# Optimization experiments

Measured on AMD Instinct MI355X. Metric: run time of the kernel, lower is better.

## Reference

```python
import jax, jax.numpy as jnp
import numpy as np
from jax.scipy.linalg import expm

D = 512      # d_model
S = 3        # num_scales
BATCH = 256
H = 8        # attention heads
HD = D // H  # head dim


def layernorm(x, g, b, eps=1e-5):
    m = jnp.mean(x, axis=-1, keepdims=True)
    v = jnp.var(x, axis=-1, keepdims=True)
    return (x - m) / jnp.sqrt(v + eps) * g + b


def setup_inputs() -> dict:
    key = jax.random.key(0)
    ks = jax.random.split(key, 16)
    sd = 1.0 / np.sqrt(D)
    inp = {
        'x': jax.random.normal(ks[0], (BATCH, D), jnp.float32),
        'h_prev': jax.random.normal(ks[1], (BATCH, D), jnp.float32),
        'lstm_h': jax.random.normal(ks[2], (S, BATCH, D), jnp.float32) * 0.1,
        'lstm_c': jax.random.normal(ks[3], (S, BATCH, D), jnp.float32) * 0.1,
        'A': jax.random.normal(ks[4], (D, D), jnp.float32) * sd,
        'Bm': jax.random.normal(ks[5], (D, D), jnp.float32) * sd,
        'dn_w1': jax.random.normal(ks[6], (D, D), jnp.float32) * sd,
        'dn_b1': jnp.zeros((D,), jnp.float32),
        'dn_g': jnp.ones((D,), jnp.float32),
        'dn_beta': jnp.zeros((D,), jnp.float32),
        'dn_w2': jax.random.normal(ks[7], (1, D), jnp.float32) * sd,
        'dn_b2': jnp.zeros((1,), jnp.float32),
        'lstm_wih': jax.random.normal(ks[8], (S, 4 * D, D), jnp.float32) * sd,
        'lstm_whh': jax.random.normal(ks[9], (S, 4 * D, D), jnp.float32) * sd,
        'lstm_bih': jnp.zeros((S, 4 * D), jnp.float32),
        'lstm_bhh': jnp.zeros((S, 4 * D), jnp.float32),
        'decays': jnp.linspace(0.5, 0.95, S, dtype=jnp.float32),
        'attn_in_w': jax.random.normal(ks[10], (3 * D, D), jnp.float32) * sd,
        'attn_in_b': jnp.zeros((3 * D,), jnp.float32),
        'attn_out_w': jax.random.normal(ks[11], (D, D), jnp.float32) * sd,
        'attn_out_b': jnp.zeros((D,), jnp.float32),
        'proj_w': jax.random.normal(ks[12], (D, (S + 2) * D), jnp.float32) * (1.0 / np.sqrt((S + 2) * D)),
        'proj_b': jnp.zeros((D,), jnp.float32),
        'proj_g': jnp.ones((D,), jnp.float32),
        'proj_beta': jnp.zeros((D,), jnp.float32),
    }
    return inp


def reference(x, h_prev, lstm_h, lstm_c, A, Bm, dn_w1, dn_b1, dn_g, dn_beta,
              dn_w2, dn_b2, lstm_wih, lstm_whh, lstm_bih, lstm_bhh, decays,
              attn_in_w, attn_in_b, attn_out_w, attn_out_b,
              proj_w, proj_b, proj_g, proj_beta):
    # ---- delta_net: Linear -> LayerNorm -> GELU(exact) -> Linear -> Softplus ----
    h1 = layernorm(x @ dn_w1.T + dn_b1, dn_g, dn_beta)
    h1 = jax.nn.gelu(h1, approximate=False)
    delta = jax.nn.softplus(h1 @ dn_w2.T + dn_b2)           # (B, 1)

    # ---- SSM update: h_t = expm(delta*A) h_prev + delta*B x ----
    A_disc = jax.vmap(expm)(delta[:, :, None] * A)          # (B, D, D)
    h_ssm = jnp.einsum('bij,bj->bi', A_disc, h_prev) + delta * jnp.einsum('ij,bj->bi', Bm, x)

    # ---- multi-scale LSTM cells (vectorized over scales) ----
    gates = (jnp.einsum('bd,skd->sbk', x, lstm_wih)
             + jnp.einsum('sbd,skd->sbk', lstm_h, lstm_whh)
             + (lstm_bih + lstm_bhh)[:, None, :])           # (S, B, 4D)
    gi, gf, gg, go = jnp.split(gates, 4, axis=-1)
    i_g = jax.nn.sigmoid(gi)
    f_g = jax.nn.sigmoid(gf)
    g_g = jnp.tanh(gg)
    o_g = jax.nn.sigmoid(go)
    c_raw = f_g * lstm_c + i_g * g_g                        # (S, B, D)
    h_new = o_g * jnp.tanh(c_raw)                           # (S, B, D)
    dec = decays[:, None, None]
    c_new = dec * lstm_c + (1.0 - dec) * c_raw              # (S, B, D)

    # ---- fusion attention: 1 query (h_ssm), S keys/values (h_new) ----
    Wq, Wk, Wv = jnp.split(attn_in_w, 3, axis=0)
    bq, bk, bv = jnp.split(attn_in_b, 3, axis=0)
    kv = jnp.transpose(h_new, (1, 0, 2))                    # (B, S, D)
    q = (h_ssm @ Wq.T + bq).reshape(-1, 1, H, HD).transpose(0, 2, 1, 3)   # (B,H,1,HD)
    k = (kv @ Wk.T + bk).reshape(-1, S, H, HD).transpose(0, 2, 1, 3)      # (B,H,S,HD)
    v = (kv @ Wv.T + bv).reshape(-1, S, H, HD).transpose(0, 2, 1, 3)
    scores = jnp.einsum('bhqe,bhke->bhqk', q, k) / np.sqrt(HD)
    attn = jax.nn.softmax(scores, axis=-1)
    ctx = jnp.einsum('bhqk,bhke->bhqe', attn, v)            # (B,H,1,HD)
    ctx = ctx.transpose(0, 2, 1, 3).reshape(-1, D)          # (B, D)
    fused = ctx @ attn_out_w.T + attn_out_b                 # (B, D)

    # ---- output projection over concat [h_ssm, fused, h_1..h_S] ----
    combined = jnp.concatenate([h_ssm, fused] + [h_new[i] for i in range(S)], axis=-1)
    output = layernorm(combined @ proj_w.T + proj_b, proj_g, proj_beta)
    return (output, h_ssm, h_new, c_new)
```

## Files before the change

kernel.cpp:

```cpp
#include <hip/hip_runtime.h>
#include <math.h>

#define DIM 512
#define NB 256
#define KMAX 12

using bf16x8 = __attribute__((ext_vector_type(8))) short;
using f32x4  = __attribute__((ext_vector_type(4))) float;
using float4v = __attribute__((ext_vector_type(4))) float;
using ushort4v = __attribute__((ext_vector_type(4))) unsigned short;

__device__ __forceinline__ unsigned short f2b(float f) {
    union { float f; unsigned int u; } v; v.f = f;
    unsigned int r = v.u + 0x7fffu + ((v.u >> 16) & 1u);
    return (unsigned short)(r >> 16);
}
__device__ __forceinline__ float b2f(unsigned short u) {
    union { unsigned int u; float f; } v; v.u = ((unsigned int)u) << 16;
    return v.f;
}
__device__ __forceinline__ ushort4v f2b4(float4v v) {
    ushort4v o;
    o.x = f2b(v.x); o.y = f2b(v.y); o.z = f2b(v.z); o.w = f2b(v.w);
    return o;
}

__device__ __forceinline__ void block_reduce2(float& s, float& q, float* sb1, float* sb2)
{
    int tid = threadIdx.x;
    #pragma unroll
    for (int off = 32; off > 0; off >>= 1) {
        s += __shfl_down(s, off);
        q += __shfl_down(q, off);
    }
    if ((tid & 63) == 0) { sb1[tid >> 6] = s; sb2[tid >> 6] = q; }
    __syncthreads();
    s = sb1[0] + sb1[1] + sb1[2] + sb1[3];
    q = sb2[0] + sb2[1] + sb2[2] + sb2[3];
    __syncthreads();
}

struct GemmDesc {
    const unsigned short* X;
    const unsigned short* W;
    const float* bias;
    float* Cf;
    unsigned short* Cb;
    unsigned short* Ct;
    int M, N, K, ldX, ldW, ldC, tr_row0, acc;
};
struct GemmArgs { GemmDesc d[10]; };
struct LnParams {
    const float* pre; const float* g; const float* beta;
    const float* w2; const float* b2; float* delta; float* coeff;
    int lnd_y;
};

__global__ __launch_bounds__(256) void gemm_mfma(GemmArgs args, LnParams lp)
{
    __shared__ unsigned short lsA[2][8192];
    __shared__ unsigned short lsB[2][8192];
    __shared__ float sb1[4], sb2[4];

    if ((int)blockIdx.y == lp.lnd_y) {
        int b = blockIdx.x, tid = threadIdx.x;
        int i0 = tid, i1 = tid + 256;
        float x0 = lp.pre[(size_t)b * DIM + i0];
        float x1 = lp.pre[(size_t)b * DIM + i1];
        float s = x0 + x1, q = x0 * x0 + x1 * x1;
        block_reduce2(s, q, sb1, sb2);
        float mean = s * (1.f / DIM);
        float var  = q * (1.f / DIM) - mean * mean;
        float inv  = rsqrtf(var + 1e-5f);
        float y0 = (x0 - mean) * inv * lp.g[i0] + lp.beta[i0];
        float y1 = (x1 - mean) * inv * lp.g[i1] + lp.beta[i1];
        float h0 = 0.5f * y0 * (1.f + erff(y0 * 0.70710678118654752f));
        float h1 = 0.5f * y1 * (1.f + erff(y1 * 0.70710678118654752f));
        float p = h0 * lp.w2[i0] + h1 * lp.w2[i1];
        float dummy = 0.f;
        block_reduce2(p, dummy, sb1, sb2);
        if (tid == 0) {
            float z = p + lp.b2[0];
            float d = (z > 20.f) ? z : log1pf(expf(z));
            lp.delta[b] = d;
            float c = 1.f;
            lp.coeff[b] = 1.f;
            for (int k = 1; k <= KMAX; ++k) { c *= d / (float)k; lp.coeff[k * 256 + b] = c; }
        }
        return;
    }

    GemmDesc de = args.d[blockIdx.y];
    int tn = de.N >> 6;
    int tiles = (de.M >> 6) * tn;
    int t = blockIdx.x;
    if (t >= tiles) return;
    int m0 = (t / tn) << 6;
    int n0 = (t % tn) << 6;

    int tid = threadIdx.x;
    int w = tid >> 6;
    int l = tid & 63;
    int nkt = de.K >> 7;

    int srow = w * 16 + (l >> 2);
    int schk = l & 3;
    const unsigned short* gA = de.X + (size_t)(m0 + srow) * de.ldX + schk * 8;
    const unsigned short* gB = de.W + (size_t)(n0 + srow) * de.ldW + schk * 8;
    unsigned short* lA = &lsA[0][(w * 64 + l) * 8];
    unsigned short* lB = &lsB[0][(w * 64 + l) * 8];

#define STAGE(bufi, kt)                                                          \
    do {                                                                         \
        for (int hh = 0; hh < 4; ++hh) {                                         \
            __builtin_amdgcn_global_load_lds(                                    \
                (const __attribute__((address_space(1))) unsigned int*)(gA + (size_t)(kt) * 128 + hh * 32), \
                (__attribute__((address_space(3))) unsigned int*)(lA + (bufi) * 8192 + hh * 2048), 16, 0, 0); \
            __builtin_amdgcn_global_load_lds(                                    \
                (const __attribute__((address_space(1))) unsigned int*)(gB + (size_t)(kt) * 128 + hh * 32), \
                (__attribute__((address_space(3))) unsigned int*)(lB + (bufi) * 8192 + hh * 2048), 16, 0, 0); \
        }                                                                        \
    } while (0)

    int mbase = (w >> 1) * 32;
    int nbase = (w & 1) * 32;

    f32x4 acc[2][2];
    #pragma unroll
    for (int i = 0; i < 2; ++i)
        #pragma unroll
        for (int j = 0; j < 2; ++j)
            acc[i][j] = (f32x4){0.f, 0.f, 0.f, 0.f};

    int kg = l >> 4;
    int fr = l & 15;
    int aslot = (mbase * 4 + fr * 4 + kg) * 8;
    int bslot = (nbase * 4 + fr * 4 + kg) * 8;

    STAGE(0, 0);

    for (int kt = 0; kt < nkt; ++kt) {
        __syncthreads();
        if (kt + 1 < nkt) STAGE((kt + 1) & 1, kt + 1);

        const unsigned short* bufA = &lsA[kt & 1][0];
        const unsigned short* bufB = &lsB[kt & 1][0];
        #pragma unroll
        for (int h = 0; h < 4; ++h) {
            bf16x8 a0 = *(const bf16x8*)(bufA + h * 2048 + aslot);
            bf16x8 a1 = *(const bf16x8*)(bufA + h * 2048 + aslot + 512);
            bf16x8 b0 = *(const bf16x8*)(bufB + h * 2048 + bslot);
            bf16x8 b1 = *(const bf16x8*)(bufB + h * 2048 + bslot + 512);
            acc[0][0] = __builtin_amdgcn_mfma_f32_16x16x32_bf16(a0, b0, acc[0][0], 0, 0, 0);
            acc[0][1] = __builtin_amdgcn_mfma_f32_16x16x32_bf16(a0, b1, acc[0][1], 0, 0, 0);
            acc[1][0] = __builtin_amdgcn_mfma_f32_16x16x32_bf16(a1, b0, acc[1][0], 0, 0, 0);
            acc[1][1] = __builtin_amdgcn_mfma_f32_16x16x32_bf16(a1, b1, acc[1][1], 0, 0, 0);
        }
    }

    #pragma unroll
    for (int mi = 0; mi < 2; ++mi) {
        #pragma unroll
        for (int ni = 0; ni < 2; ++ni) {
            int col = n0 + nbase + ni * 16 + fr;
            float bv = de.bias ? de.bias[col] : 0.f;
            #pragma unroll
            for (int r = 0; r < 4; ++r) {
                int row = m0 + mbase + mi * 16 + (l >> 4) * 4 + r;
                float v = acc[mi][ni][r] + bv;
                if (de.Cf) {
                    if (de.acc == 2)      atomicAdd(&de.Cf[(size_t)row * de.ldC + col], v);
                    else if (de.acc == 1) de.Cf[(size_t)row * de.ldC + col] += v;
                    else                  de.Cf[(size_t)row * de.ldC + col] = v;
                } else {
                    de.Cb[(size_t)row * de.ldC + col] = f2b(v);
                }
                if (de.Ct && row >= de.tr_row0)
                    de.Ct[(size_t)col * 512 + (row - de.tr_row0)] = f2b(v);
            }
        }
    }
#undef STAGE
}

#define NSEG 13
struct PrepArgs {
    const float* sA[NSEG]; const float* sB[NSEG]; unsigned short* dst[NSEG];
    int n4[NSEG], dRL4[NSEG], sRLA4[NSEG], sRLB4[NSEG], half4[NSEG], offA[NSEG];
    const float* A; unsigned short* ATb;
    const float* W2src; unsigned short* W2dst;
};
__global__ __launch_bounds__(256) void prep_kernel(PrepArgs a)
{
    __shared__ float tile[32][33];
    int bid = blockIdx.x, tid = threadIdx.x;
    if (bid < 2048) {
        const int gstride = 2048 * 256;
        int g0 = bid * 256 + tid;
        for (int seg = 0; seg < NSEG; ++seg) {
            int n4 = a.n4[seg];
            const float* sA = a.sA[seg];
            const float* sB = a.sB[seg];
            unsigned short* d = a.dst[seg];
            int dRL4 = a.dRL4[seg], sRLA4 = a.sRLA4[seg], sRLB4 = a.sRLB4[seg];
            int half4 = a.half4[seg], offA = a.offA[seg];
            for (int i = g0; i < n4; i += gstride) {
                int r = i / dRL4, c = i - r * dRL4;
                const float* src = (c < half4)
                    ? sA + ((size_t)r * sRLA4 + offA + c) * 4
                    : sB + ((size_t)r * sRLB4 + (c - half4)) * 4;
                float4v v = *(const float4v*)src;
                *(ushort4v*)(d + (size_t)i * 4) = f2b4(v);
            }
        }
    } else {
        int tt = bid - 2048;
        const float* src = a.A;
        unsigned short* dst = a.ATb;
        if (tt >= 256) { tt -= 256; src = a.W2src; dst = a.W2dst; }
        int bx = tt & 15, by = tt >> 4;
        int tx = tid & 31, ty = tid >> 5;
        #pragma unroll
        for (int i = 0; i < 32; i += 8)
            tile[ty + i][tx] = src[(size_t)(by * 32 + ty + i) * 512 + bx * 32 + tx];
        __syncthreads();
        #pragma unroll
        for (int i = 0; i < 32; i += 8)
            dst[(size_t)(bx * 32 + ty + i) * 512 + by * 32 + tx] = f2b(tile[tx][ty + i]);
    }
}

__global__ void pointwise_fused(
    const float* __restrict__ Tm, const float* __restrict__ coeff,
    const float* __restrict__ h_prev, const float* __restrict__ delta,
    const float* __restrict__ Bx, float* __restrict__ hssm,
    unsigned short* __restrict__ combb,
    const float* __restrict__ gates, const float* __restrict__ bih,
    const float* __restrict__ bhh, const float* __restrict__ cin,
    const float* __restrict__ decays,
    float* __restrict__ hout, float* __restrict__ cout,
    const unsigned short* __restrict__ P2b, const float* __restrict__ aout_b,
    const float* __restrict__ proj_b, float* __restrict__ pbc)
{
    int idx4 = blockIdx.x * 256 + threadIdx.x;
    int base = idx4 * 4;
    if (base < 131072) {
        int b = base >> 9, i = base & 511;
        const float* Tr = Tm + (size_t)b * (KMAX * DIM) + i;
        float4v a = *(const float4v*)(h_prev + base);
        #pragma unroll
        for (int k = 1; k <= KMAX; ++k) {
            float c = coeff[k * 256 + b];
            float4v t = *(const float4v*)(Tr + (size_t)(k - 1) * DIM);
            a.x += c * t.x; a.y += c * t.y; a.z += c * t.z; a.w += c * t.w;
        }
        float dl = delta[b];
        float4v bx = *(const float4v*)(Bx + base);
        a.x += dl * bx.x; a.y += dl * bx.y; a.z += dl * bx.z; a.w += dl * bx.w;
        *(float4v*)(hssm + base) = a;
        *(ushort4v*)(combb + (size_t)b * 2048 + i) = f2b4(a);
    } else if (base < 524288) {
        int i2 = base - 131072;
        int s = i2 / (NB * DIM);
        int r = i2 - s * (NB * DIM);
        int b = r >> 9, d = r & 511;
        const float* gr = gates + (size_t)s * 524288 + (size_t)b * 2048 + d;
        const float* bi = bih + s * 2048 + d;
        const float* bh = bhh + s * 2048 + d;
        float4v gi = *(const float4v*)(gr);
        float4v gf = *(const float4v*)(gr + 512);
        float4v gg = *(const float4v*)(gr + 1024);
        float4v go = *(const float4v*)(gr + 1536);
        float4v bi0 = *(const float4v*)(bi),        bh0 = *(const float4v*)(bh);
        float4v bi1 = *(const float4v*)(bi + 512),  bh1 = *(const float4v*)(bh + 512);
        float4v bi2 = *(const float4v*)(bi + 1024), bh2 = *(const float4v*)(bh + 1024);
        float4v bi3 = *(const float4v*)(bi + 1536), bh3 = *(const float4v*)(bh + 1536);
        float4v c = *(const float4v*)(cin + i2);
        float dec = decays[s];
        float4v hn, cn;
        #pragma unroll
        for (int j = 0; j < 4; ++j) {
            float vgi = ((const float*)&gi)[j] + ((const float*)&bi0)[j] + ((const float*)&bh0)[j];
            float vgf = ((const float*)&gf)[j] + ((const float*)&bi1)[j] + ((const float*)&bh1)[j];
            float vgg = ((const float*)&gg)[j] + ((const float*)&bi2)[j] + ((const float*)&bh2)[j];
            float vgo = ((const float*)&go)[j] + ((const float*)&bi3)[j] + ((const float*)&bh3)[j];
            float ig = 1.f / (1.f + expf(-vgi));
            float fg = 1.f / (1.f + expf(-vgf));
            float g_ = tanhf(vgg);
            float og = 1.f / (1.f + expf(-vgo));
            float cc = ((const float*)&c)[j];
            float craw = fg * cc + ig * g_;
            ((float*)&hn)[j] = og * tanhf(craw);
            ((float*)&cn)[j] = dec * cc + (1.f - dec) * craw;
        }
        *(float4v*)(hout + i2) = hn;
        *(float4v*)(cout + i2) = cn;
        *(ushort4v*)(combb + (size_t)b * 2048 + 512 + s * 512 + d) = f2b4(hn);
    } else {
        int ii = idx4 - 131072;
        const unsigned short* pr = P2b + (size_t)ii * 512;
        float acc = 0.f;
        for (int k = 0; k < 512; k += 8) {
            ushort4v w0 = *(const ushort4v*)(pr + k);
            ushort4v w1 = *(const ushort4v*)(pr + k + 4);
            float4v a0 = *(const float4v*)(aout_b + k);
            float4v a1 = *(const float4v*)(aout_b + k + 4);
            acc += a0.x * b2f(w0.x) + a0.y * b2f(w0.y)
                 + a0.z * b2f(w0.z) + a0.w * b2f(w0.w)
                 + a1.x * b2f(w1.x) + a1.y * b2f(w1.y)
                 + a1.z * b2f(w1.z) + a1.w * b2f(w1.w);
        }
        pbc[ii] = proj_b[ii] + acc;
    }
}

__global__ __launch_bounds__(256) void tail_kernel(
    const unsigned short* __restrict__ qb, const unsigned short* __restrict__ kvb,
    const unsigned short* __restrict__ M2b, const float* __restrict__ projA,
    const float* __restrict__ fin_g, const float* __restrict__ fin_beta,
    float* __restrict__ outp)
{
    __shared__ float ctxs[512];
    __shared__ float sb1[4], sb2[4];
    int b = blockIdx.x, tid = threadIdx.x;

    if (tid < 128) {
        int h = tid >> 4, sub = (tid & 15) * 4;
        int col = h * 64 + sub;
        ushort4v q4 = *(const ushort4v*)(qb + (size_t)b * 512 + col);
        float qf[4] = { b2f(q4.x), b2f(q4.y), b2f(q4.z), b2f(q4.w) };
        float p[3];
        ushort4v k4[3], v4[3];
        #pragma unroll
        for (int s = 0; s < 3; ++s) {
            k4[s] = *(const ushort4v*)(kvb + (size_t)s * 262144 + (size_t)b * 1024 + col);
            v4[s] = *(const ushort4v*)(kvb + (size_t)s * 262144 + (size_t)b * 1024 + 512 + col);
            p[s] = qf[0] * b2f(k4[s].x) + qf[1] * b2f(k4[s].y)
                 + qf[2] * b2f(k4[s].z) + qf[3] * b2f(k4[s].w);
        }
        #pragma unroll
        for (int off = 1; off < 16; off <<= 1) {
            p[0] += __shfl_xor(p[0], off);
            p[1] += __shfl_xor(p[1], off);
            p[2] += __shfl_xor(p[2], off);
        }
        const float scale = 0.125f;
        float p0 = p[0] * scale, p1 = p[1] * scale, p2 = p[2] * scale;
        float m = fmaxf(p0, fmaxf(p1, p2));
        float w0 = expf(p0 - m), w1 = expf(p1 - m), w2 = expf(p2 - m);
        float invs = 1.f / (w0 + w1 + w2);
        ctxs[col + 0] = (w0 * b2f(v4[0].x) + w1 * b2f(v4[1].x) + w2 * b2f(v4[2].x)) * invs;
        ctxs[col + 1] = (w0 * b2f(v4[0].y) + w1 * b2f(v4[1].y) + w2 * b2f(v4[2].y)) * invs;
        ctxs[col + 2] = (w0 * b2f(v4[0].z) + w1 * b2f(v4[1].z) + w2 * b2f(v4[2].z)) * invs;
        ctxs[col + 3] = (w0 * b2f(v4[0].w) + w1 * b2f(v4[1].w) + w2 * b2f(v4[2].w)) * invs;
    }
    __syncthreads();

    float x0 = projA[(size_t)b * 512 + tid];
    float x1 = projA[(size_t)b * 512 + tid + 256];
    {
        const unsigned short* mr0 = M2b + (size_t)tid * 512;
        const unsigned short* mr1 = M2b + (size_t)(tid + 256) * 512;
        for (int k = 0; k < 512; k += 8) {
            ushort4v a0 = *(const ushort4v*)(mr0 + k);
            ushort4v a1 = *(const ushort4v*)(mr0 + k + 4);
            ushort4v c0 = *(const ushort4v*)(mr1 + k);
            ushort4v c1 = *(const ushort4v*)(mr1 + k + 4);
            float t0 = ctxs[k+0], t1 = ctxs[k+1], t2 = ctxs[k+2], t3 = ctxs[k+3];
            float t4 = ctxs[k+4], t5 = ctxs[k+5], t6 = ctxs[k+6], t7 = ctxs[k+7];
            x0 += t0*b2f(a0.x) + t1*b2f(a0.y) + t2*b2f(a0.z) + t3*b2f(a0.w)
                + t4*b2f(a1.x) + t5*b2f(a1.y) + t6*b2f(a1.z) + t7*b2f(a1.w);
            x1 += t0*b2f(c0.x) + t1*b2f(c0.y) + t2*b2f(c0.z) + t3*b2f(c0.w)
                + t4*b2f(c1.x) + t5*b2f(c1.y) + t6*b2f(c1.z) + t7*b2f(c1.w);
        }
    }

    float s = x0 + x1, q = x0 * x0 + x1 * x1;
    block_reduce2(s, q, sb1, sb2);
    float mean = s * (1.f / DIM);
    float var  = q * (1.f / DIM) - mean * mean;
    float inv  = rsqrtf(var + 1e-5f);
    outp[(size_t)b * DIM + tid]       = (x0 - mean) * inv * fin_g[tid]       + fin_beta[tid];
    outp[(size_t)b * DIM + tid + 256] = (x1 - mean) * inv * fin_g[tid + 256] + fin_beta[tid + 256];
}

extern "C" void kernel_launch(void* const* d_in, const int* in_sizes, int n_in,
                              void* d_out, int out_size, void* d_ws, size_t ws_size,
                              hipStream_t stream)
{
    const float* x        = (const float*)d_in[0];
    const float* h_prev   = (const float*)d_in[1];
    const float* lstm_h   = (const float*)d_in[2];
    const float* lstm_c   = (const float*)d_in[3];
    const float* A        = (const float*)d_in[4];
    const float* Bm       = (const float*)d_in[5];
    const float* dn_w1    = (const float*)d_in[6];
    const float* dn_b1    = (const float*)d_in[7];
    const float* dn_g     = (const float*)d_in[8];
    const float* dn_beta  = (const float*)d_in[9];
    const float* dn_w2    = (const float*)d_in[10];
    const float* dn_b2    = (const float*)d_in[11];
    const float* wih      = (const float*)d_in[12];
    const float* whh      = (const float*)d_in[13];
    const float* bih      = (const float*)d_in[14];
    const float* bhh      = (const float*)d_in[15];
    const float* decays   = (const float*)d_in[16];
    const float* ain_w    = (const float*)d_in[17];
    const float* ain_b    = (const float*)d_in[18];
    const float* aout_w   = (const float*)d_in[19];
    const float* aout_b   = (const float*)d_in[20];
    const float* proj_w   = (const float*)d_in[21];
    const float* proj_b   = (const float*)d_in[22];
    const float* proj_g   = (const float*)d_in[23];
    const float* proj_bt  = (const float*)d_in[24];

    float* out  = (float*)d_out;
    float* hssm = out + 131072;
    float* hnew = out + 262144;
    float* cnew = out + 655360;

    unsigned short* us = (unsigned short*)d_ws;
    unsigned short* hpb     = us;
    unsigned short* ATb     = us + 131072;
    unsigned short* dn_w1b  = us + 393216;
    unsigned short* Bmb     = us + 655360;
    unsigned short* ain_wb  = us + 917504;
    unsigned short* proj_wb = us + 1703936;
    unsigned short* P2b     = us + 2752512;
    unsigned short* aout_wTb= us + 3014656;
    unsigned short* Pw      = us + 3276800;
    unsigned short* Qa      = us + 5373952;
    unsigned short* Qb      = us + 5636096;
    unsigned short* Wcat    = us + 5898240;
    unsigned short* Xcat    = us + 12189696;
    unsigned short* combb   = us + 12976128;
    unsigned short* qb      = us + 13500416;
    unsigned short* kvb     = us + 13631488;
    unsigned short* U8b     = us + 14417920;
    float* fbase  = (float*)(us + 14548992);
    float* pre1   = fbase;
    float* delta  = fbase + 131072;
    float* coeff  = fbase + 131328;
    float* Bx     = fbase + 134656;
    float* Tm     = fbase + 265728;
    float* gates  = fbase + 1838592;
    float* pbc    = fbase + 3411456;
    unsigned short* M2b = (unsigned short*)(fbase + 3412480);
    float* projout = pre1;

    LnParams lpOff; lpOff.pre = nullptr; lpOff.g = nullptr; lpOff.beta = nullptr;
    lpOff.w2 = nullptr; lpOff.b2 = nullptr; lpOff.delta = nullptr; lpOff.coeff = nullptr;
    lpOff.lnd_y = -1;

    PrepArgs pa;
    int sidx = 0;
    auto LIN = [&](const float* s, unsigned short* d, int n4) {
        pa.sA[sidx]=s; pa.sB[sidx]=s; pa.dst[sidx]=d; pa.n4[sidx]=n4;
        pa.dRL4[sidx]=n4; pa.sRLA4[sidx]=0; pa.sRLB4[sidx]=0;
        pa.half4[sidx]=n4; pa.offA[sidx]=0; ++sidx;
    };
    LIN(h_prev, hpb,     32768);
    LIN(A,      Pw,      65536);
    LIN(dn_w1,  dn_w1b,  65536);
    LIN(Bm,     Bmb,     65536);
    LIN(ain_w,  ain_wb,  196608);
    pa.sA[sidx]=proj_w; pa.sB[sidx]=proj_w + 1024; pa.dst[sidx]=proj_wb; pa.n4[sidx]=262144;
    pa.dRL4[sidx]=512; pa.sRLA4[sidx]=640; pa.sRLB4[sidx]=640; pa.half4[sidx]=128; pa.offA[sidx]=0; ++sidx;
    pa.sA[sidx]=proj_w; pa.sB[sidx]=proj_w; pa.dst[sidx]=P2b; pa.n4[sidx]=65536;
    pa.dRL4[sidx]=128; pa.sRLA4[sidx]=640; pa.sRLB4[sidx]=640; pa.half4[sidx]=128; pa.offA[sidx]=128; ++sidx;
    for (int s = 0; s < 3; ++s) {
        pa.sA[sidx]=wih + (size_t)s*1048576; pa.sB[sidx]=whh + (size_t)s*1048576;
        pa.dst[sidx]=Wcat + (size_t)s*2097152; pa.n4[sidx]=524288;
        pa.dRL4[sidx]=256; pa.sRLA4[sidx]=128; pa.sRLB4[sidx]=128; pa.half4[sidx]=128; pa.offA[sidx]=0; ++sidx;
    }
    for (int s = 0; s < 3; ++s) {
        pa.sA[sidx]=x; pa.sB[sidx]=lstm_h + (size_t)s*131072;
        pa.dst[sidx]=Xcat + (size_t)s*262144; pa.n4[sidx]=65536;
        pa.dRL4[sidx]=256; pa.sRLA4[sidx]=128; pa.sRLB4[sidx]=128; pa.half4[sidx]=128; pa.offA[sidx]=0; ++sidx;
    }
    pa.A = A; pa.ATb = ATb;
    pa.W2src = aout_w; pa.W2dst = aout_wTb;
    prep_kernel<<<2560, 256, 0, stream>>>(pa);

    GemmArgs ga;
    ga.d[0] = { Xcat, dn_w1b, dn_b1, pre1, nullptr, nullptr, 256, 512, 512, 1024, 512, 512, 0, 0 };
    ga.d[1] = { Xcat, Bmb,    nullptr, Bx,  nullptr, nullptr, 256, 512, 512, 1024, 512, 512, 0, 0 };
    ga.d[2] = { Pw, ATb, nullptr, nullptr, Pw + 1*262144, Qa, 512, 512, 512, 512, 512, 512, 0, 0 };
    for (int s = 0; s < 3; ++s)
        ga.d[3 + s] = { Xcat + (size_t)s * 262144, Wcat + (size_t)s * 2097152, nullptr,
                        gates + (size_t)s * 524288, nullptr, nullptr,
                        256, 2048, 1024, 1024, 1024, 2048, 0, 0 };
    ga.d[6] = { P2b, aout_wTb, nullptr, nullptr, M2b, nullptr, 512, 512, 512, 512, 512, 512, 0, 0 };
    gemm_mfma<<<dim3(128, 7), 256, 0, stream>>>(ga, lpOff);

    LnParams lp1 = { pre1, dn_g, dn_beta, dn_w2, dn_b2, delta, coeff, 1 };
    ga.d[0] = { Pw, Qa, nullptr, nullptr, Pw + 2*262144, Qb, 1024, 512, 512, 512, 512, 512, 512, 0 };
    gemm_mfma<<<dim3(256, 2), 256, 0, stream>>>(ga, lp1);

    ga.d[0] = { Pw, Qb, nullptr, nullptr, Pw + 4*262144, nullptr, 2048, 512, 512, 512, 512, 512, 0, 0 };
    gemm_mfma<<<dim3(256, 1), 256, 0, stream>>>(ga, lpOff);

    ga.d[0] = { hpb, Pw, nullptr, Tm, nullptr, nullptr, 256, 4096, 512, 512, 512, 6144, 0, 0 };
    ga.d[1] = { hpb, Pw + 7*262144, nullptr, nullptr, U8b, nullptr, 256, 512, 512, 512, 512, 512, 0, 0 };
    gemm_mfma<<<dim3(256, 2), 256, 0, stream>>>(ga, lpOff);

    ga.d[0] = { U8b, Pw, nullptr, Tm + 4096, nullptr, nullptr, 256, 2048, 512, 512, 512, 6144, 0, 0 };
    gemm_mfma<<<dim3(128, 1), 256, 0, stream>>>(ga, lpOff);

    pointwise_fused<<<514, 256, 0, stream>>>(Tm, coeff, h_prev, delta, Bx, hssm, combb,
                                             gates, bih, bhh, lstm_c, decays, hnew, cnew,
                                             P2b, aout_b, proj_b, pbc);

    ga.d[0] = { combb, ain_wb, ain_b, nullptr, qb, nullptr, 256, 512, 512, 2048, 512, 512, 0, 0 };
    for (int s = 0; s < 3; ++s)
        ga.d[1 + s] = { combb + 512 + (size_t)s * 512, ain_wb + 262144, ain_b + 512,
                        nullptr, kvb + (size_t)s * 262144, nullptr, 256, 1024, 512, 2048, 512, 1024, 0, 0 };
    ga.d[4] = { combb, proj_wb, pbc, projout, nullptr, nullptr, 256, 512, 2048, 2048, 2048, 512, 0, 0 };
    gemm_mfma<<<dim3(64, 5), 256, 0, stream>>>(ga, lpOff);

    tail_kernel<<<256, 256, 0, stream>>>(qb, kvb, M2b, projout,
                                         proj_g, proj_bt, out);
}
```

Measured before the change: 230.3 us.

## Fuse LSTM cell epilogue into gates GEMM, remap tiles across XCDs, move bias precompute

Reorders the LSTM weight rows during bf16 prep so each 64-column GEMM tile holds the i/f/g/o gates for the same 16 hidden units. The gates GEMM can then apply the LSTM cell update in its epilogue through a shared-memory tile, instead of writing the full fp32 gates buffer and reading it back in the pointwise kernel. Tile indices are also remapped so that consecutive tiles land on the same XCD, which is meant to improve L2 locality. The proj-bias/attn-out-bias precompute moves into spare blocks of the prep kernel using fp32 weights. The costs are an extra LDS round-trip and a strided epilogue with 4 gate columns per thread in place of vectorised float4 access.

```diff
diff --git a/kernel.cpp b/kernel.cpp
--- a/kernel.cpp
+++ b/kernel.cpp
@@ -49,11 +49,13 @@
     unsigned short* Ct;
     int M, N, K, ldX, ldW, ldC, tr_row0, acc;
 };
-struct GemmArgs { GemmDesc d[10]; };
+struct GemmArgs { GemmDesc d[8]; };
 struct LnParams {
     const float* pre; const float* g; const float* beta;
     const float* w2; const float* b2; float* delta; float* coeff;
     int lnd_y;
+    const float* cin; const float* bih; const float* bhh; const float* decays;
+    float* hout; float* cout; unsigned short* combb;
 };
 
 __global__ __launch_bounds__(256) void gemm_mfma(GemmArgs args, LnParams lp)
@@ -91,12 +93,15 @@
     }
 
     GemmDesc de = args.d[blockIdx.y];
-    int tn = de.N >> 6;
-    int tiles = (de.M >> 6) * tn;
+    int tmm = de.M >> 6;
+    int tiles = tmm * (de.N >> 6);
     int t = blockIdx.x;
     if (t >= tiles) return;
-    int m0 = (t / tn) << 6;
-    int n0 = (t % tn) << 6;
+    int qc = tiles >> 3, rc = tiles & 7;
+    int xcd = t & 7, li = t >> 3;
+    int tt = (xcd < rc) ? (xcd * (qc + 1) + li) : (rc * (qc + 1) + (xcd - rc) * qc + li);
+    int m0 = (tt % tmm) << 6;
+    int n0 = (tt / tmm) << 6;
 
     int tid = threadIdx.x;
     int w = tid >> 6;
@@ -156,6 +161,46 @@
             acc[1][0] = __builtin_amdgcn_mfma_f32_16x16x32_bf16(a1, b0, acc[1][0], 0, 0, 0);
             acc[1][1] = __builtin_amdgcn_mfma_f32_16x16x32_bf16(a1, b1, acc[1][1], 0, 0, 0);
         }
+    }
+
+    if (de.acc == 3) {
+        __syncthreads();
+        float* tile = (float*)lsA;
+        #pragma unroll
+        for (int mi = 0; mi < 2; ++mi)
+            #pragma unroll
+            for (int ni = 0; ni < 2; ++ni) {
+                int ct = nbase + ni * 16 + fr;
+                #pragma unroll
+                for (int r = 0; r < 4; ++r) {
+                    int rt = mbase + mi * 16 + kg * 4 + r;
+                    tile[rt * 65 + ct] = acc[mi][ni][r];
+                }
+            }
+        __syncthreads();
+        int s = de.tr_row0;
+        int d0 = n0 >> 2;
+        float dec = lp.decays[s];
+        for (int cell = tid; cell < 1024; cell += 256) {
+            int row = cell >> 4, dsub = cell & 15;
+            int d = d0 + dsub;
+            int b = m0 + row;
+            float vgi = tile[row * 65 +      dsub] + lp.bih[s * 2048 +        d] + lp.bhh[s * 2048 +        d];
+            float vgf = tile[row * 65 + 16 + dsub] + lp.bih[s * 2048 +  512 + d] + lp.bhh[s * 2048 +  512 + d];
+            float vgg = tile[row * 65 + 32 + dsub] + lp.bih[s * 2048 + 1024 + d] + lp.bhh[s * 2048 + 1024 + d];
+            float vgo = tile[row * 65 + 48 + dsub] + lp.bih[s * 2048 + 1536 + d] + lp.bhh[s * 2048 + 1536 + d];
+            float cc = lp.cin[(size_t)s * 131072 + (size_t)b * 512 + d];
+            float ig = 1.f / (1.f + expf(-vgi));
+            float fg = 1.f / (1.f + expf(-vgf));
+            float g_ = tanhf(vgg);
+            float og = 1.f / (1.f + expf(-vgo));
+            float craw = fg * cc + ig * g_;
+            float hn = og * tanhf(craw);
+            lp.hout[(size_t)s * 131072 + (size_t)b * 512 + d] = hn;
+            lp.cout[(size_t)s * 131072 + (size_t)b * 512 + d] = dec * cc + (1.f - dec) * craw;
+            lp.combb[(size_t)b * 2048 + 512 + s * 512 + d] = f2b(hn);
+        }
+        return;
     }
 
     #pragma unroll
@@ -186,9 +231,10 @@
 #define NSEG 13
 struct PrepArgs {
     const float* sA[NSEG]; const float* sB[NSEG]; unsigned short* dst[NSEG];
-    int n4[NSEG], dRL4[NSEG], sRLA4[NSEG], sRLB4[NSEG], half4[NSEG], offA[NSEG];
+    int n4[NSEG], dRL4[NSEG], sRLA4[NSEG], sRLB4[NSEG], half4[NSEG], offA[NSEG], gmap[NSEG];
     const float* A; unsigned short* ATb;
     const float* W2src; unsigned short* W2dst;
+    const float* projw; const float* projb; const float* aoutb; float* pbc;
 };
 __global__ __launch_bounds__(256) void prep_kernel(PrepArgs a)
 {
@@ -203,17 +249,18 @@
             const float* sB = a.sB[seg];
             unsigned short* d = a.dst[seg];
             int dRL4 = a.dRL4[seg], sRLA4 = a.sRLA4[seg], sRLB4 = a.sRLB4[seg];
-            int half4 = a.half4[seg], offA = a.offA[seg];
+            int half4 = a.half4[seg], offA = a.offA[seg], gm = a.gmap[seg];
             for (int i = g0; i < n4; i += gstride) {
                 int r = i / dRL4, c = i - r * dRL4;
+                int rs = gm ? (((r >> 4) & 3) * 512 + ((r >> 6) << 4) + (r & 15)) : r;
                 const float* src = (c < half4)
-                    ? sA + ((size_t)r * sRLA4 + offA + c) * 4
-                    : sB + ((size_t)r * sRLB4 + (c - half4)) * 4;
+                    ? sA + ((size_t)rs * sRLA4 + offA + c) * 4
+                    : sB + ((size_t)rs * sRLB4 + (c - half4)) * 4;
                 float4v v = *(const float4v*)src;
                 *(ushort4v*)(d + (size_t)i * 4) = f2b4(v);
             }
         }
-    } else {
+    } else if (bid < 2560) {
         int tt = bid - 2048;
         const float* src = a.A;
         unsigned short* dst = a.ATb;
@@ -227,6 +274,16 @@
         #pragma unroll
         for (int i = 0; i < 32; i += 8)
             dst[(size_t)(bx * 32 + ty + i) * 512 + by * 32 + tx] = f2b(tile[tx][ty + i]);
+    } else {
+        int i = (bid - 2560) * 256 + tid;
+        const float* pr = a.projw + (size_t)i * 2560 + 512;
+        float acc = 0.f;
+        for (int j = 0; j < 512; j += 4) {
+            float4v w = *(const float4v*)(pr + j);
+            float4v ab = *(const float4v*)(a.aoutb + j);
+            acc += w.x * ab.x + w.y * ab.y + w.z * ab.z + w.w * ab.w;
+        }
+        a.pbc[i] = a.projb[i] + acc;
     }
 }
 
@@ -234,84 +291,24 @@
     const float* __restrict__ Tm, const float* __restrict__ coeff,
     const float* __restrict__ h_prev, const float* __restrict__ delta,
     const float* __restrict__ Bx, float* __restrict__ hssm,
-    unsigned short* __restrict__ combb,
-    const float* __restrict__ gates, const float* __restrict__ bih,
-    const float* __restrict__ bhh, const float* __restrict__ cin,
-    const float* __restrict__ decays,
-    float* __restrict__ hout, float* __restrict__ cout,
-    const unsigned short* __restrict__ P2b, const float* __restrict__ aout_b,
-    const float* __restrict__ proj_b, float* __restrict__ pbc)
+    unsigned short* __restrict__ combb)
 {
     int idx4 = blockIdx.x * 256 + threadIdx.x;
     int base = idx4 * 4;
-    if (base < 131072) {
-        int b = base >> 9, i = base & 511;
-        const float* Tr = Tm + (size_t)b * (KMAX * DIM) + i;
-        float4v a = *(const float4v*)(h_prev + base);
-        #pragma unroll
-        for (int k = 1; k <= KMAX; ++k) {
-            float c = coeff[k * 256 + b];
-            float4v t = *(const float4v*)(Tr + (size_t)(k - 1) * DIM);
-            a.x += c * t.x; a.y += c * t.y; a.z += c * t.z; a.w += c * t.w;
-        }
-        float dl = delta[b];
-        float4v bx = *(const float4v*)(Bx + base);
-        a.x += dl * bx.x; a.y += dl * bx.y; a.z += dl * bx.z; a.w += dl * bx.w;
-        *(float4v*)(hssm + base) = a;
-        *(ushort4v*)(combb + (size_t)b * 2048 + i) = f2b4(a);
-    } else if (base < 524288) {
-        int i2 = base - 131072;
-        int s = i2 / (NB * DIM);
-        int r = i2 - s * (NB * DIM);
-        int b = r >> 9, d = r & 511;
-        const float* gr = gates + (size_t)s * 524288 + (size_t)b * 2048 + d;
-        const float* bi = bih + s * 2048 + d;
-        const float* bh = bhh + s * 2048 + d;
-        float4v gi = *(const float4v*)(gr);
-        float4v gf = *(const float4v*)(gr + 512);
-        float4v gg = *(const float4v*)(gr + 1024);
-        float4v go = *(const float4v*)(gr + 1536);
-        float4v bi0 = *(const float4v*)(bi),        bh0 = *(const float4v*)(bh);
-        float4v bi1 = *(const float4v*)(bi + 512),  bh1 = *(const float4v*)(bh + 512);
-        float4v bi2 = *(const float4v*)(bi + 1024), bh2 = *(const float4v*)(bh + 1024);
-        float4v bi3 = *(const float4v*)(bi + 1536), bh3 = *(const float4v*)(bh + 1536);
-        float4v c = *(const float4v*)(cin + i2);
-        float dec = decays[s];
-        float4v hn, cn;
-        #pragma unroll
-        for (int j = 0; j < 4; ++j) {
-            float vgi = ((const float*)&gi)[j] + ((const float*)&bi0)[j] + ((const float*)&bh0)[j];
-            float vgf = ((const float*)&gf)[j] + ((const float*)&bi1)[j] + ((const float*)&bh1)[j];
-            float vgg = ((const float*)&gg)[j] + ((const float*)&bi2)[j] + ((const float*)&bh2)[j];
-            float vgo = ((const float*)&go)[j] + ((const float*)&bi3)[j] + ((const float*)&bh3)[j];
-            float ig = 1.f / (1.f + expf(-vgi));
-            float fg = 1.f / (1.f + expf(-vgf));
-            float g_ = tanhf(vgg);
-            float og = 1.f / (1.f + expf(-vgo));
-            float cc = ((const float*)&c)[j];
-            float craw = fg * cc + ig * g_;
-            ((float*)&hn)[j] = og * tanhf(craw);
-            ((float*)&cn)[j] = dec * cc + (1.f - dec) * craw;
-        }
-        *(float4v*)(hout + i2) = hn;
-        *(float4v*)(cout + i2) = cn;
-        *(ushort4v*)(combb + (size_t)b * 2048 + 512 + s * 512 + d) = f2b4(hn);
-    } else {
-        int ii = idx4 - 131072;
-        const unsigned short* pr = P2b + (size_t)ii * 512;
-        float acc = 0.f;
-        for (int k = 0; k < 512; k += 8) {
-            ushort4v w0 = *(const ushort4v*)(pr + k);
-            ushort4v w1 = *(const ushort4v*)(pr + k + 4);
-            float4v a0 = *(const float4v*)(aout_b + k);
-            float4v a1 = *(const float4v*)(aout_b + k + 4);
-            acc += a0.x * b2f(w0.x) + a0.y * b2f(w0.y)
-                 + a0.z * b2f(w0.z) + a0.w * b2f(w0.w)
-                 + a1.x * b2f(w1.x) + a1.y * b2f(w1.y)
-                 + a1.z * b2f(w1.z) + a1.w * b2f(w1.w);
-        }
-        pbc[ii] = proj_b[ii] + acc;
-    }
+    int b = base >> 9, i = base & 511;
+    const float* Tr = Tm + (size_t)b * (KMAX * DIM) + i;
+    float4v a = *(const float4v*)(h_prev + base);
+    #pragma unroll
+    for (int k = 1; k <= KMAX; ++k) {
+        float c = coeff[k * 256 + b];
+        float4v t = *(const float4v*)(Tr + (size_t)(k - 1) * DIM);
+        a.x += c * t.x; a.y += c * t.y; a.z += c * t.z; a.w += c * t.w;
+    }
+    float dl = delta[b];
+    float4v bx = *(const float4v*)(Bx + base);
+    a.x += dl * bx.x; a.y += dl * bx.y; a.z += dl * bx.z; a.w += dl * bx.w;
+    *(float4v*)(hssm + base) = a;
+    *(ushort4v*)(combb + (size_t)b * 2048 + i) = f2b4(a);
 }
 
 __global__ __launch_bounds__(256) void tail_kernel(
@@ -443,21 +440,23 @@
     float* coeff  = fbase + 131328;
     float* Bx     = fbase + 134656;
     float* Tm     = fbase + 265728;
-    float* gates  = fbase + 1838592;
-    float* pbc    = fbase + 3411456;
-    unsigned short* M2b = (unsigned short*)(fbase + 3412480);
+    float* pbc    = fbase + 1838592;
+    unsigned short* M2b = (unsigned short*)(fbase + 1839616);
     float* projout = pre1;
 
-    LnParams lpOff; lpOff.pre = nullptr; lpOff.g = nullptr; lpOff.beta = nullptr;
+    LnParams lpOff;
+    lpOff.pre = nullptr; lpOff.g = nullptr; lpOff.beta = nullptr;
     lpOff.w2 = nullptr; lpOff.b2 = nullptr; lpOff.delta = nullptr; lpOff.coeff = nullptr;
     lpOff.lnd_y = -1;
+    lpOff.cin = lstm_c; lpOff.bih = bih; lpOff.bhh = bhh; lpOff.decays = decays;
+    lpOff.hout = hnew; lpOff.cout = cnew; lpOff.combb = combb;
 
     PrepArgs pa;
     int sidx = 0;
     auto LIN = [&](const float* s, unsigned short* d, int n4) {
         pa.sA[sidx]=s; pa.sB[sidx]=s; pa.dst[sidx]=d; pa.n4[sidx]=n4;
         pa.dRL4[sidx]=n4; pa.sRLA4[sidx]=0; pa.sRLB4[sidx]=0;
-        pa.half4[sidx]=n4; pa.offA[sidx]=0; ++sidx;
+        pa.half4[sidx]=n4; pa.offA[sidx]=0; pa.gmap[sidx]=0; ++sidx;
     };
     LIN(h_prev, hpb,     32768);
     LIN(A,      Pw,      65536);
@@ -465,22 +464,25 @@
     LIN(Bm,     Bmb,     65536);
     LIN(ain_w,  ain_wb,  196608);
     pa.sA[sidx]=proj_w; pa.sB[sidx]=proj_w + 1024; pa.dst[sidx]=proj_wb; pa.n4[sidx]=262144;
-    pa.dRL4[sidx]=512; pa.sRLA4[sidx]=640; pa.sRLB4[sidx]=640; pa.half4[sidx]=128; pa.offA[sidx]=0; ++sidx;
+    pa.dRL4[sidx]=512; pa.sRLA4[sidx]=640; pa.sRLB4[sidx]=640; pa.half4[sidx]=128; pa.offA[sidx]=0; pa.gmap[sidx]=0; ++sidx;
     pa.sA[sidx]=proj_w; pa.sB[sidx]=proj_w; pa.dst[sidx]=P2b; pa.n4[sidx]=65536;
-    pa.dRL4[sidx]=128; pa.sRLA4[sidx]=640; pa.sRLB4[sidx]=640; pa.half4[sidx]=128; pa.offA[sidx]=128; ++sidx;
+    pa.dRL4[sidx]=128; pa.sRLA4[sidx]=640; pa.sRLB4[sidx]=640; pa.half4[sidx]=128; pa.offA[sidx]=128; pa.gmap[sidx]=0; ++sidx;
     for (int s = 0; s < 3; ++s) {
         pa.sA[sidx]=wih + (size_t)s*1048576; pa.sB[sidx]=whh + (size_t)s*1048576;
         pa.dst[sidx]=Wcat + (size_t)s*2097152; pa.n4[sidx]=524288;
-        pa.dRL4[sidx]=256; pa.sRLA4[sidx]=128; pa.sRLB4[sidx]=128; pa.half4[sidx]=128; pa.offA[sidx]=0; ++sidx;
+        pa.dRL4[sidx]=256; pa.sRLA4[sidx]=128; pa.sRLB4[sidx]=128; pa.half4[sidx]=128; pa.offA[sidx]=0;
+        pa.gmap[sidx]=1; ++sidx;
     }
     for (int s = 0; s < 3; ++s) {
         pa.sA[sidx]=x; pa.sB[sidx]=lstm_h + (size_t)s*131072;
         pa.dst[sidx]=Xcat + (size_t)s*262144; pa.n4[sidx]=65536;
-        pa.dRL4[sidx]=256; pa.sRLA4[sidx]=128; pa.sRLB4[sidx]=128; pa.half4[sidx]=128; pa.offA[sidx]=0; ++sidx;
+        pa.dRL4[sidx]=256; pa.sRLA4[sidx]=128; pa.sRLB4[sidx]=128; pa.half4[sidx]=128; pa.offA[sidx]=0;
+        pa.gmap[sidx]=0; ++sidx;
     }
     pa.A = A; pa.ATb = ATb;
     pa.W2src = aout_w; pa.W2dst = aout_wTb;
-    prep_kernel<<<2560, 256, 0, stream>>>(pa);
+    pa.projw = proj_w; pa.projb = proj_b; pa.aoutb = aout_b; pa.pbc = pbc;
+    prep_kernel<<<2562, 256, 0, stream>>>(pa);
 
     GemmArgs ga;
     ga.d[0] = { Xcat, dn_w1b, dn_b1, pre1, nullptr, nullptr, 256, 512, 512, 1024, 512, 512, 0, 0 };
@@ -488,12 +490,14 @@
     ga.d[2] = { Pw, ATb, nullptr, nullptr, Pw + 1*262144, Qa, 512, 512, 512, 512, 512, 512, 0, 0 };
     for (int s = 0; s < 3; ++s)
         ga.d[3 + s] = { Xcat + (size_t)s * 262144, Wcat + (size_t)s * 2097152, nullptr,
-                        gates + (size_t)s * 524288, nullptr, nullptr,
-                        256, 2048, 1024, 1024, 1024, 2048, 0, 0 };
+                        nullptr, nullptr, nullptr,
+                        256, 2048, 1024, 1024, 1024, 2048, s, 3 };
     ga.d[6] = { P2b, aout_wTb, nullptr, nullptr, M2b, nullptr, 512, 512, 512, 512, 512, 512, 0, 0 };
     gemm_mfma<<<dim3(128, 7), 256, 0, stream>>>(ga, lpOff);
 
-    LnParams lp1 = { pre1, dn_g, dn_beta, dn_w2, dn_b2, delta, coeff, 1 };
+    LnParams lp1 = lpOff;
+    lp1.pre = pre1; lp1.g = dn_g; lp1.beta = dn_beta; lp1.w2 = dn_w2; lp1.b2 = dn_b2;
+    lp1.delta = delta; lp1.coeff = coeff; lp1.lnd_y = 1;
     ga.d[0] = { Pw, Qa, nullptr, nullptr, Pw + 2*262144, Qb, 1024, 512, 512, 512, 512, 512, 512, 0 };
     gemm_mfma<<<dim3(256, 2), 256, 0, stream>>>(ga, lp1);
 
@@ -507,9 +511,7 @@
     ga.d[0] = { U8b, Pw, nullptr, Tm + 4096, nullptr, nullptr, 256, 2048, 512, 512, 512, 6144, 0, 0 };
     gemm_mfma<<<dim3(128, 1), 256, 0, stream>>>(ga, lpOff);
 
-    pointwise_fused<<<514, 256, 0, stream>>>(Tm, coeff, h_prev, delta, Bx, hssm, combb,
-                                             gates, bih, bhh, lstm_c, decays, hnew, cnew,
-                                             P2b, aout_b, proj_b, pbc);
+    pointwise_fused<<<128, 256, 0, stream>>>(Tm, coeff, h_prev, delta, Bx, hssm, combb);
 
     ga.d[0] = { combb, ain_wb, ain_b, nullptr, qb, nullptr, 256, 512, 512, 2048, 512, 512, 0, 0 };
     for (int s = 0; s < 3; ++s)
```

After: 233.4 us. About the same (+1.4%).
